# Performance work log

Hardware: AMD Instinct MI355X
Metric: run time of the kernel (lower is better)

The kernel has to match this reference:

```python
import jax, jax.numpy as jnp
import numpy as np

BINS = 50
MIN_V = 0.0
MAX_V = 1.0
SIGMA = 10.0
DELTA = (MAX_V - MIN_V) / BINS
EPS = 1e-8


def _soft_bin(v, centers):
    # v: [N, D] -> [N, bins, D]
    d = v[:, None, :] - centers[None, :, None]
    return jax.nn.sigmoid(SIGMA * (d + DELTA / 2)) - jax.nn.sigmoid(SIGMA * (d - DELTA / 2))


def setup_inputs() -> dict:
    key = jax.random.key(0)
    k1, k2 = jax.random.split(key)
    im1 = jax.random.uniform(k1, (8, 384, 384), dtype=jnp.float32)
    im2 = jax.random.uniform(k2, (8, 384, 384), dtype=jnp.float32)
    return {"im1": im1, "im2": im2}


def reference(im1, im2):
    n = im1.shape[0]
    x = im1.reshape(n, -1)
    y = im2.reshape(n, -1)
    centers = MIN_V + DELTA * (jnp.arange(BINS, dtype=jnp.float32) + 0.5)
    xs = _soft_bin(x, centers)  # [N, bins, D]
    ys = _soft_bin(y, centers)  # [N, bins, D]
    hgram = jnp.einsum('nbd,ncd->nbc', xs, ys)  # [N, bins, bins]
    # NOTE: original normalizes by the sum over the WHOLE batch
    p_xy = hgram / jnp.sum(hgram)
    marginal_x = jnp.sum(p_xy, axis=2)  # [N, bins]
    marginal_y = jnp.sum(p_xy, axis=1)  # [N, bins]
    joined = marginal_x[:, :, None] * marginal_y[:, None, :]  # [N, bins, bins]
    mi_per = jnp.sum(
        p_xy * (jnp.log(p_xy + EPS) - jnp.log(joined + EPS)), axis=(1, 2)
    )
    return jnp.sum(mi_per)  # reduction='sum'
```

## Files before the change

### kernel.cpp

```cpp
#include <hip/hip_runtime.h>


#define D_TOTAL   147456
#define NBATCH    8
#define BINS      50
#define NEDGE     28
#define KSLICES   96
#define KC        256
#define SLICE_LEN (D_TOTAL / KSLICES)
#define ITERS     (SLICE_LEN / KC)
#define LDS_STR   280

typedef _Float16 half8  __attribute__((ext_vector_type(8)));
typedef __fp16   fp16x2 __attribute__((ext_vector_type(2)));
typedef float    f32x16 __attribute__((ext_vector_type(16)));

struct Tab { float c[NEDGE]; };
constexpr Tab make_tab() {
    Tab t{};
    double c = 0.6703200460356393;
    const double lam = 1.4918246976412703;
    for (int i = 0; i < NEDGE; ++i) { t.c[i] = (float)c; c *= lam; }
    return t;
}
constexpr Tab TAB = make_tab();

__global__ __launch_bounds__(256, 3) void hgram_kernel(const float* __restrict__ im1,
                                                       const float* __restrict__ im2,
                                                       float* __restrict__ hg,
                                                       float* __restrict__ out) {
    __shared__ __align__(16) _Float16 Xs[32][LDS_STR];
    __shared__ __align__(16) _Float16 Ys[32][LDS_STR];

    const int tid   = threadIdx.x;
    const int slice = blockIdx.x;
    const int n     = blockIdx.y;
    const int base  = n * D_TOTAL + slice * SLICE_LEN;

    if (slice == 0 && n == 0 && tid == 0) out[0] = 0.f;

    {
        unsigned* px = (unsigned*)&Xs[28][0];
        unsigned* py = (unsigned*)&Ys[28][0];
        for (int i = tid; i < 4 * LDS_STR / 2; i += 256) { px[i] = 0u; py[i] = 0u; }
    }

    const int h    = tid & 127;
    const int isY  = tid >> 7;
    const float2* src2 = (const float2*)((isY ? im2 : im1) + base);
    _Float16* plane = isY ? &Ys[0][0] : &Xs[0][0];
    _Float16* dst   = plane + 2 * h;

    const int lane  = tid & 63;
    const int w     = tid >> 6;
    const int kw    = w << 6;
    const int row32 = lane & 31;
    const int kg    = (lane >> 5) << 3;

    f32x16 acc = {0.f,0.f,0.f,0.f,0.f,0.f,0.f,0.f,
                  0.f,0.f,0.f,0.f,0.f,0.f,0.f,0.f};

    float2 v = src2[h];
    for (int it = 0; it < ITERS; ++it) {
        float2 nv = {0.f, 0.f};
        if (it + 1 < ITERS) nv = src2[(it + 1) * (KC / 2) + h];
        {
            const float Ea = __builtin_amdgcn_exp2f(v.x * -14.426950408889634f);
            const float Eb = __builtin_amdgcn_exp2f(v.y * -14.426950408889634f);
            #pragma unroll
            for (int i = 0; i < NEDGE; ++i) {
                const float c = TAB.c[i];
                float ta = __builtin_amdgcn_rcpf(__builtin_fmaf(c * Ea, 0.00390625f, 0.00390625f));
                float tb = __builtin_amdgcn_rcpf(__builtin_fmaf(c * Eb, 0.00390625f, 0.00390625f));
                fp16x2 p = __builtin_amdgcn_cvt_pkrtz(ta, tb);
                *(fp16x2*)(dst + i * LDS_STR) = p;
            }
        }
        __syncthreads();
        #pragma unroll
        for (int s = 0; s < 4; ++s) {
            const int k0 = kw + s * 16 + kg;
            half8 a = *(const half8*)&Xs[row32][k0];
            half8 b = *(const half8*)&Ys[row32][k0];
            acc = __builtin_amdgcn_mfma_f32_32x32x16_f16(a, b, acc, 0, 0, 0);
        }
        __syncthreads();
        v = nv;
    }

    float* const Pf = (float*)&Xs[0][0];
    {
        float* Pw = Pf + (w << 10);
        const int prow_base = (lane >> 5) << 2;
        #pragma unroll
        for (int reg = 0; reg < 16; ++reg) {
            const int prow = (reg & 3) + ((reg >> 2) << 3) + prow_base;
            Pw[prow * 32 + row32] = acc[reg];
        }
    }
    __syncthreads();

    float* hgn = hg + n * 1024;
    for (int e = tid; e < 1024; e += 256) {
        const int r = e >> 5, c = e & 31;
        if (r < NEDGE && c < NEDGE) {
            float s = Pf[e] + Pf[1024 + e] + Pf[2048 + e] + Pf[3072 + e];
            atomicAdd(&hgn[e], s);
        }
    }
}

__global__ __launch_bounds__(1024) void finalize_kernel(const float* __restrict__ hg,
                                                        float* __restrict__ out) {
    __shared__ float Gs[NEDGE][29];
    __shared__ float mx[BINS], my[BINS];
    __shared__ float red[16];
    __shared__ float sT;
    const int tid = threadIdx.x;
    const int n   = blockIdx.x;
    const float* hgn = hg + n * 1024;

    for (int idx = tid; idx < NEDGE * NEDGE; idx += 1024) {
        int r = idx / NEDGE, c = idx - r * NEDGE;
        Gs[r][c] = hgn[r * 32 + c];
    }
    if (tid == 0) {
        float t = 0.f;
        #pragma unroll
        for (int b = 0; b < NBATCH; ++b) {
            const float* p = hg + b * 1024;
            t += p[1 * 32 + 1] - p[1 * 32 + 26] - p[26 * 32 + 1] + p[26 * 32 + 26];
        }
        sT = t;
    }
    __syncthreads();

    if (tid < 2 * BINS) {
        const int which = (tid >= BINS) ? 1 : 0;
        const int b = which ? tid - BINS : tid;
        const int q = b >> 1;
        float w0, w1, w2, w3;
        if (b & 1) { w0 = -1.f; w1 = 9.f; w2 = -7.f; w3 = -1.f; }
        else       { w0 =  1.f; w1 = 7.f; w2 = -9.f; w3 =  1.f; }
        float m;
        if (which == 0) {
            m = w0 * (Gs[q][1]   - Gs[q][26])
              + w1 * (Gs[q+1][1] - Gs[q+1][26])
              + w2 * (Gs[q+2][1] - Gs[q+2][26])
              + w3 * (Gs[q+3][1] - Gs[q+3][26]);
            mx[b] = m * 0.0625f;
        } else {
            m = w0 * (Gs[1][q]   - Gs[26][q])
              + w1 * (Gs[1][q+1] - Gs[26][q+1])
              + w2 * (Gs[1][q+2] - Gs[26][q+2])
              + w3 * (Gs[1][q+3] - Gs[26][q+3]);
            my[b] = m * 0.0625f;
        }
    }
    __syncthreads();

    const float invT = 1.0f / sT;
    const float invT2 = invT * invT;
    float mi = 0.f;
    for (int task = tid; task < 25 * 25; task += 1024) {
        const int bp = task / 25, cp = task - bp * 25;
        float g[4][4];
        #pragma unroll
        for (int r = 0; r < 4; ++r)
            #pragma unroll
            for (int s = 0; s < 4; ++s) g[r][s] = Gs[bp + r][cp + s];
        float rde[4], rdo[4];
        #pragma unroll
        for (int r = 0; r < 4; ++r) {
            rde[r] =  g[r][0] + 7.f * g[r][1] - 9.f * g[r][2] + g[r][3];
            rdo[r] = -g[r][0] + 9.f * g[r][1] - 7.f * g[r][2] - g[r][3];
        }
        const float hee = ( rde[0] + 7.f*rde[1] - 9.f*rde[2] + rde[3]) * (1.f/256.f);
        const float heo = ( rdo[0] + 7.f*rdo[1] - 9.f*rdo[2] + rdo[3]) * (1.f/256.f);
        const float hoe = (-rde[0] + 9.f*rde[1] - 7.f*rde[2] - rde[3]) * (1.f/256.f);
        const float hoo = (-rdo[0] + 9.f*rdo[1] - 7.f*rdo[2] - rdo[3]) * (1.f/256.f);
        const int b0 = 2 * bp, c0 = 2 * cp;
        {
            float p = hee * invT, jo = mx[b0] * my[c0] * invT2;
            mi += p * (__logf(p + 1e-8f) - __logf(jo + 1e-8f));
        }
        {
            float p = heo * invT, jo = mx[b0] * my[c0 + 1] * invT2;
            mi += p * (__logf(p + 1e-8f) - __logf(jo + 1e-8f));
        }
        {
            float p = hoe * invT, jo = mx[b0 + 1] * my[c0] * invT2;
            mi += p * (__logf(p + 1e-8f) - __logf(jo + 1e-8f));
        }
        {
            float p = hoo * invT, jo = mx[b0 + 1] * my[c0 + 1] * invT2;
            mi += p * (__logf(p + 1e-8f) - __logf(jo + 1e-8f));
        }
    }
    #pragma unroll
    for (int o = 32; o > 0; o >>= 1) mi += __shfl_down(mi, o, 64);
    if ((tid & 63) == 0) red[tid >> 6] = mi;
    __syncthreads();
    if (tid == 0) {
        float t = 0.f;
        #pragma unroll
        for (int i = 0; i < 16; ++i) t += red[i];
        atomicAdd(&out[0], t);
    }
}

extern "C" void kernel_launch(void* const* d_in, const int* in_sizes, int n_in,
                              void* d_out, int out_size, void* d_ws, size_t ws_size,
                              hipStream_t stream) {
    const float* im1 = (const float*)d_in[0];
    const float* im2 = (const float*)d_in[1];
    float* out = (float*)d_out;
    float* hg  = (float*)d_ws;

    (void)hipMemsetAsync(d_ws, 0, NBATCH * 1024 * sizeof(float), stream);
    hgram_kernel<<<dim3(KSLICES, NBATCH), dim3(256), 0, stream>>>(im1, im2, hg, out);
    finalize_kernel<<<dim3(NBATCH), dim3(1024), 0, stream>>>(hg, out);
}
```

Measured before the change: 75.22 us.

## Replace atomic histogram accumulation with per-slice partials reduced in finalize

Each hgram block now writes its full 32x32 partial histogram to a per-slice workspace slot instead of atomically adding into a shared per-batch histogram. The finalize kernel sums the 96 slice partials per entry, and computes the global normalization total from the corner partials across all batches. This removes the memset launch and atomic contention, at the cost of more workspace traffic (8x96x4KB) and a longer serial reduction loop in finalize.

```diff
diff --git a/kernel.cpp b/kernel.cpp
--- a/kernel.cpp
+++ b/kernel.cpp
@@ -27,7 +27,7 @@
 
 __global__ __launch_bounds__(256, 3) void hgram_kernel(const float* __restrict__ im1,
                                                        const float* __restrict__ im2,
-                                                       float* __restrict__ hg,
+                                                       float* __restrict__ hgp,
                                                        float* __restrict__ out) {
     __shared__ __align__(16) _Float16 Xs[32][LDS_STR];
     __shared__ __align__(16) _Float16 Ys[32][LDS_STR];
@@ -100,36 +100,53 @@
     }
     __syncthreads();
 
-    float* hgn = hg + n * 1024;
-    for (int e = tid; e < 1024; e += 256) {
-        const int r = e >> 5, c = e & 31;
-        if (r < NEDGE && c < NEDGE) {
-            float s = Pf[e] + Pf[1024 + e] + Pf[2048 + e] + Pf[3072 + e];
-            atomicAdd(&hgn[e], s);
-        }
-    }
-}
-
-__global__ __launch_bounds__(1024) void finalize_kernel(const float* __restrict__ hg,
+    float* hp = hgp + (n * KSLICES + slice) * 1024;
+    #pragma unroll
+    for (int k = 0; k < 4; ++k) {
+        const int e = tid + k * 256;
+        hp[e] = Pf[e] + Pf[1024 + e] + Pf[2048 + e] + Pf[3072 + e];
+    }
+}
+
+__global__ __launch_bounds__(1024) void finalize_kernel(const float* __restrict__ hgp,
                                                         float* __restrict__ out) {
     __shared__ float Gs[NEDGE][29];
     __shared__ float mx[BINS], my[BINS];
+    __shared__ float ct[32];
     __shared__ float red[16];
     __shared__ float sT;
     const int tid = threadIdx.x;
     const int n   = blockIdx.x;
-    const float* hgn = hg + n * 1024;
-
-    for (int idx = tid; idx < NEDGE * NEDGE; idx += 1024) {
-        int r = idx / NEDGE, c = idx - r * NEDGE;
-        Gs[r][c] = hgn[r * 32 + c];
-    }
+
+    {
+        const int r = tid >> 5, c = tid & 31;
+        if (r < NEDGE && c < NEDGE) {
+            const float* p = hgp + n * (KSLICES * 1024) + tid;
+            float s = 0.f;
+            #pragma unroll 8
+            for (int sl = 0; sl < KSLICES; ++sl) s += p[sl * 1024];
+            Gs[r][c] = s;
+        }
+    }
+    {
+        const int pr = tid >> 5;
+        const int j  = tid & 31;
+        const int b  = pr >> 2;
+        const int cn = pr & 3;
+        const int cidx = (cn < 2 ? 32 : 832) + ((cn & 1) ? 26 : 1);
+        const float* p = hgp + b * (KSLICES * 1024) + cidx;
+        float vv = p[j * 1024] + p[(j + 32) * 1024] + p[(j + 64) * 1024];
+        #pragma unroll
+        for (int o = 16; o > 0; o >>= 1) vv += __shfl_down(vv, o, 32);
+        if (j == 0) ct[pr] = vv;
+    }
+    __syncthreads();
     if (tid == 0) {
         float t = 0.f;
         #pragma unroll
-        for (int b = 0; b < NBATCH; ++b) {
-            const float* p = hg + b * 1024;
-            t += p[1 * 32 + 1] - p[1 * 32 + 26] - p[26 * 32 + 1] + p[26 * 32 + 26];
+        for (int pr = 0; pr < 32; ++pr) {
+            const int cn = pr & 3;
+            t += ((cn == 0 || cn == 3) ? 1.f : -1.f) * ct[pr];
         }
         sT = t;
     }
@@ -215,9 +232,8 @@
     const float* im1 = (const float*)d_in[0];
     const float* im2 = (const float*)d_in[1];
     float* out = (float*)d_out;
-    float* hg  = (float*)d_ws;
-
-    (void)hipMemsetAsync(d_ws, 0, NBATCH * 1024 * sizeof(float), stream);
-    hgram_kernel<<<dim3(KSLICES, NBATCH), dim3(256), 0, stream>>>(im1, im2, hg, out);
-    finalize_kernel<<<dim3(NBATCH), dim3(1024), 0, stream>>>(hg, out);
-}
+    float* hgp = (float*)d_ws;
+
+    hgram_kernel<<<dim3(KSLICES, NBATCH), dim3(256), 0, stream>>>(im1, im2, hgp, out);
+    finalize_kernel<<<dim3(NBATCH), dim3(1024), 0, stream>>>(hgp, out);
+}
```

Result: slower. 79.11 us (+5.2%).
